# Optimization experiments

Hardware: AMD Instinct MI355X
Metric: run time of the kernel (lower is better)

The kernel has to match this reference:

```python
import jax, jax.numpy as jnp
import numpy as np

B, H, W, C = 16, 64, 64, 256
DIM = 256

def setup_inputs() -> dict:
    key = jax.random.key(0)
    ks = jax.random.split(key, 9)
    s_in = 1.0 / np.sqrt(C)
    x = jax.random.normal(ks[0], (B, H, W, C), dtype=jnp.float32)
    Wq = jax.random.normal(ks[1], (C, DIM), dtype=jnp.float32) * s_in
    bq = jnp.zeros((DIM,), dtype=jnp.float32)
    Wk = jax.random.normal(ks[2], (C, DIM), dtype=jnp.float32) * s_in
    bk = jnp.zeros((DIM,), dtype=jnp.float32)
    Wv = jax.random.normal(ks[3], (C, DIM), dtype=jnp.float32) * s_in
    bv = jnp.zeros((DIM,), dtype=jnp.float32)
    # 'out' conv sees 1 input channel (after the channel reduce_sum)
    Wo = jax.random.normal(ks[4], (1, DIM), dtype=jnp.float32)
    bo = jnp.zeros((DIM,), dtype=jnp.float32)
    return {"x": x, "Wq": Wq, "bq": bq, "Wk": Wk, "bk": bk,
            "Wv": Wv, "bv": bv, "Wo": Wo, "bo": bo}

def reference(x, Wq, bq, Wk, bk, Wv, bv, Wo, bo):
    # 1x1 convs == channel GEMMs
    q = jnp.einsum('bhwc,cd->bhwd', x, Wq) + bq
    k = jnp.einsum('bhwc,cd->bhwd', x, Wk) + bk
    v = jnp.einsum('bhwc,cd->bhwd', x, Wv) + bv
    # channel-reduce score -> [B,H,W,1], softmax jointly over spatial axes
    score = jnp.sum(q * k, axis=-1, keepdims=True)
    attn = jax.nn.softmax(score, axis=(1, 2))
    # channel-reduce of v weighted by per-pixel attn -> [B,H,W,1]
    out = jnp.sum(v * attn, axis=-1, keepdims=True)
    # final 1x1 conv: 1 input channel -> DIM output channels
    return jnp.einsum('bhwc,cd->bhwd', out, Wo) + bo
```

## Files before the change

kernel.cpp:

```cpp
#include <hip/hip_runtime.h>


typedef __bf16 bf16_t;
typedef __attribute__((ext_vector_type(8))) __bf16 bf16x8;
typedef __attribute__((ext_vector_type(4))) __bf16 bf16x4;
typedef __attribute__((ext_vector_type(4))) float f32x4;

#define NBATCH 16
#define NPIX   65536
#define PPB    4096

#define MH_OFF    0u
#define ML_OFF    131072u
#define U_OFF     262144u
#define WV_OFF    263168u
#define SCL_OFF   264192u
#define SCORE_OFF 264448u
#define SV_OFF    526592u
#define BMAX_OFF  788736u
#define BSUM_OFF  788800u

__global__ __launch_bounds__(256) void prep_kernel(
    const float* __restrict__ Wq, const float* __restrict__ bq,
    const float* __restrict__ Wk, const float* __restrict__ bk,
    const float* __restrict__ Wv, const float* __restrict__ bv,
    bf16_t* __restrict__ Mh, bf16_t* __restrict__ Ml,
    float* __restrict__ u, float* __restrict__ wv, float* __restrict__ scl)
{
    const int t = threadIdx.x;
    if (blockIdx.x < 256) {
        const int c = blockIdx.x;
        __shared__ __align__(16) float wq_row[256];
        wq_row[t] = Wq[c * 256 + t];
        __syncthreads();
        const float4* wk4 = (const float4*)(Wk + t * 256);
        const float4* wq4 = (const float4*)wq_row;
        float acc = 0.f;
#pragma unroll 8
        for (int i = 0; i < 64; ++i) {
            float4 a = wq4[i], b = wk4[i];
            acc += a.x * b.x + a.y * b.y + a.z * b.z + a.w * b.w;
        }
        bf16_t h = (bf16_t)acc;
        float hf = (float)h;
        bf16_t l = (bf16_t)(acc - hf);
        Mh[c * 256 + t] = h;
        Ml[c * 256 + t] = l;
    } else {
        float uacc = 0.f, wvacc = 0.f;
        const float* wqr = Wq + t * 256;
        const float* wkr = Wk + t * 256;
        const float* wvr = Wv + t * 256;
#pragma unroll 4
        for (int d = 0; d < 256; ++d) {
            uacc += wqr[d] * bk[d] + wkr[d] * bq[d];
            wvacc += wvr[d];
        }
        u[t] = uacc;
        wv[t] = wvacc;
        __shared__ float r1[256], r2[256];
        r1[t] = bq[t] * bk[t];
        r2[t] = bv[t];
        __syncthreads();
        for (int s = 128; s > 0; s >>= 1) {
            if (t < s) { r1[t] += r1[t + s]; r2[t] += r2[t + s]; }
            __syncthreads();
        }
        if (t == 0) { scl[0] = r1[0]; scl[1] = r2[0]; }
    }
}

__device__ __forceinline__ int swz(int row, int col) {
    return row * 256 + (col ^ ((row & 7) << 3));
}

__global__ __launch_bounds__(256, 2) void score_kernel(
    const float* __restrict__ x,
    const bf16_t* __restrict__ Mh, const bf16_t* __restrict__ Ml,
    const float* __restrict__ u, const float* __restrict__ wvp,
    const float* __restrict__ scl,
    float* __restrict__ score, float* __restrict__ svout)
{
    __shared__ __align__(16) char smem[65536];
    bf16_t* Ah = (bf16_t*)smem;
    bf16_t* Al = Ah + 16384;
    float* redS = (float*)smem;
    float* redV = redS + 256;

    const int t = threadIdx.x;
    const int lane = t & 63;
    const int wid = t >> 6;
    const int l15 = lane & 15;
    const int lg = lane >> 4;
    const int pix0 = blockIdx.x * 64;
    const int wcol0 = wid * 64;

#pragma unroll
    for (int i = 0; i < 16; ++i) {
        int chunk = i * 256 + t;
        int r = chunk >> 6;
        int c4 = (chunk & 63) << 2;
        float4 xv = *(const float4*)(x + (size_t)(pix0 + r) * 256 + c4);
        bf16x4 hi, lo;
        hi[0] = (bf16_t)xv.x; hi[1] = (bf16_t)xv.y;
        hi[2] = (bf16_t)xv.z; hi[3] = (bf16_t)xv.w;
        lo[0] = (bf16_t)(xv.x - (float)hi[0]);
        lo[1] = (bf16_t)(xv.y - (float)hi[1]);
        lo[2] = (bf16_t)(xv.z - (float)hi[2]);
        lo[3] = (bf16_t)(xv.w - (float)hi[3]);
        int idx = swz(r, c4);
        *(bf16x4*)&Ah[idx] = hi;
        *(bf16x4*)&Al[idx] = lo;
    }
    __syncthreads();

    f32x4 acc[4][4];
#pragma unroll
    for (int i = 0; i < 4; ++i)
#pragma unroll
        for (int j = 0; j < 4; ++j)
            acc[i][j] = (f32x4){0.f, 0.f, 0.f, 0.f};

#pragma unroll
    for (int ks = 0; ks < 8; ++ks) {
        const int k0 = ks * 32;
        bf16x8 af_h[4], af_l[4];
#pragma unroll
        for (int rf = 0; rf < 4; ++rf) {
            int row = rf * 16 + l15;
            int idx = swz(row, k0 + lg * 8);
            af_h[rf] = *(const bf16x8*)&Ah[idx];
            af_l[rf] = *(const bf16x8*)&Al[idx];
        }
        bf16x8 bfr_h[4], bfr_l[4];
#pragma unroll
        for (int cf = 0; cf < 4; ++cf) {
            int col = wcol0 + cf * 16 + l15;
            size_t boff = (size_t)col * 256 + k0 + lg * 8;
            bfr_h[cf] = *(const bf16x8*)(Mh + boff);
            bfr_l[cf] = *(const bf16x8*)(Ml + boff);
        }
#pragma unroll
        for (int rf = 0; rf < 4; ++rf)
#pragma unroll
            for (int cf = 0; cf < 4; ++cf)
                acc[rf][cf] = __builtin_amdgcn_mfma_f32_16x16x32_bf16(
                    af_h[rf], bfr_h[cf], acc[rf][cf], 0, 0, 0);
#pragma unroll
        for (int rf = 0; rf < 4; ++rf)
#pragma unroll
            for (int cf = 0; cf < 4; ++cf)
                acc[rf][cf] = __builtin_amdgcn_mfma_f32_16x16x32_bf16(
                    af_l[rf], bfr_h[cf], acc[rf][cf], 0, 0, 0);
#pragma unroll
        for (int rf = 0; rf < 4; ++rf)
#pragma unroll
            for (int cf = 0; cf < 4; ++cf)
                acc[rf][cf] = __builtin_amdgcn_mfma_f32_16x16x32_bf16(
                    af_h[rf], bfr_l[cf], acc[rf][cf], 0, 0, 0);
    }

    float uu[4], wvl[4];
#pragma unroll
    for (int cf = 0; cf < 4; ++cf) {
        uu[cf] = u[wcol0 + cf * 16 + l15];
        wvl[cf] = wvp[wcol0 + cf * 16 + l15];
    }
    float sacc[4][4], vacc[4][4];
#pragma unroll
    for (int rf = 0; rf < 4; ++rf) {
#pragma unroll
        for (int r = 0; r < 4; ++r) {
            int row = rf * 16 + lg * 4 + r;
            float s = 0.f, v = 0.f;
#pragma unroll
            for (int cf = 0; cf < 4; ++cf) {
                int col = wcol0 + cf * 16 + l15;
                int idx = swz(row, col);
                float xv = (float)Ah[idx] + (float)Al[idx];
                s += xv * (acc[rf][cf][r] + uu[cf]);
                v += xv * wvl[cf];
            }
#pragma unroll
            for (int m = 1; m < 16; m <<= 1) {
                s += __shfl_xor(s, m, 64);
                v += __shfl_xor(v, m, 64);
            }
            sacc[rf][r] = s;
            vacc[rf][r] = v;
        }
    }
    __syncthreads();
    if (l15 == 0) {
#pragma unroll
        for (int rf = 0; rf < 4; ++rf)
#pragma unroll
            for (int r = 0; r < 4; ++r) {
                int row = rf * 16 + lg * 4 + r;
                redS[wid * 64 + row] = sacc[rf][r];
                redV[wid * 64 + row] = vacc[rf][r];
            }
    }
    __syncthreads();
    if (t < 64) {
        float c0 = scl[0], bvs = scl[1];
        float s = redS[t] + redS[64 + t] + redS[128 + t] + redS[192 + t] + c0;
        float v = redV[t] + redV[64 + t] + redV[128 + t] + redV[192 + t] + bvs;
        score[pix0 + t] = s;
        svout[pix0 + t] = v;
    }
}

__global__ __launch_bounds__(256) void stats_kernel(
    const float* __restrict__ score,
    float* __restrict__ bmax, float* __restrict__ bsum)
{
    const int b = blockIdx.x, t = threadIdx.x;
    const float* s = score + b * PPB;
    __shared__ float red[256];
    float m = -1e30f;
    for (int i = t; i < PPB; i += 256) m = fmaxf(m, s[i]);
    red[t] = m;
    __syncthreads();
    for (int k = 128; k > 0; k >>= 1) {
        if (t < k) red[t] = fmaxf(red[t], red[t + k]);
        __syncthreads();
    }
    m = red[0];
    __syncthreads();
    float sum = 0.f;
    for (int i = t; i < PPB; i += 256) sum += __expf(s[i] - m);
    red[t] = sum;
    __syncthreads();
    for (int k = 128; k > 0; k >>= 1) {
        if (t < k) red[t] += red[t + k];
        __syncthreads();
    }
    if (t == 0) { bmax[b] = m; bsum[b] = red[0]; }
}

__global__ __launch_bounds__(256) void out_kernel(
    const float* __restrict__ score, const float* __restrict__ sv,
    const float* __restrict__ bmax, const float* __restrict__ bsum,
    const float* __restrict__ Wo, const float* __restrict__ bo,
    float* __restrict__ out)
{
    const int total = NPIX * 64;
    const int stride = gridDim.x * blockDim.x;
    for (int idx = blockIdx.x * blockDim.x + threadIdx.x; idx < total; idx += stride) {
        int p = idx >> 6;
        int c4 = (idx & 63) << 2;
        int b = p >> 12;
        float g = __expf(score[p] - bmax[b]) / bsum[b] * sv[p];
        float4 w = *(const float4*)(Wo + c4);
        float4 bb = *(const float4*)(bo + c4);
        float4 o = { g * w.x + bb.x, g * w.y + bb.y, g * w.z + bb.z, g * w.w + bb.w };
        *(float4*)(out + (size_t)p * 256 + c4) = o;
    }
}

extern "C" void kernel_launch(void* const* d_in, const int* in_sizes, int n_in,
                              void* d_out, int out_size, void* d_ws, size_t ws_size,
                              hipStream_t stream) {
    const float* x  = (const float*)d_in[0];
    const float* Wq = (const float*)d_in[1];
    const float* bq = (const float*)d_in[2];
    const float* Wk = (const float*)d_in[3];
    const float* bk = (const float*)d_in[4];
    const float* Wv = (const float*)d_in[5];
    const float* bv = (const float*)d_in[6];
    const float* Wo = (const float*)d_in[7];
    const float* bo = (const float*)d_in[8];
    float* out = (float*)d_out;
    char* ws = (char*)d_ws;

    bf16_t* Mh = (bf16_t*)(ws + MH_OFF);
    bf16_t* Ml = (bf16_t*)(ws + ML_OFF);
    float* u   = (float*)(ws + U_OFF);
    float* wv  = (float*)(ws + WV_OFF);
    float* scl = (float*)(ws + SCL_OFF);
    float* score = (float*)(ws + SCORE_OFF);
    float* sv    = (float*)(ws + SV_OFF);
    float* bmax  = (float*)(ws + BMAX_OFF);
    float* bsum  = (float*)(ws + BSUM_OFF);

    prep_kernel<<<dim3(257), dim3(256), 0, stream>>>(Wq, bq, Wk, bk, Wv, bv, Mh, Ml, u, wv, scl);
    score_kernel<<<dim3(NPIX / 64), dim3(256), 0, stream>>>(x, Mh, Ml, u, wv, scl, score, sv);
    stats_kernel<<<dim3(NBATCH), dim3(256), 0, stream>>>(score, bmax, bsum);
    out_kernel<<<dim3(2048), dim3(256), 0, stream>>>(score, sv, bmax, bsum, Wo, bo, out);
}
```

Baseline: 102.6 us.

## Split score kernel into two K-halves with 8 waves and overlapped loads

The score kernel now runs 512 threads (8 waves, 32 output columns each) and loads x in two 128-channel halves, so the second half's global load and conversion can overlap the first half's MFMA work. The linear terms x·u and x·wv are computed directly from fp32 x during staging rather than after the GEMM, and the 3-pass MFMA is interleaved per tile. The stats kernel becomes a single-pass online softmax reduction using vectorized loads and wave shuffles, and the output kernel gets twice as many blocks. The risks are more register pressure from holding a second x half in registers, and a higher occupancy hint that may not be reachable with 64KB of LDS per block.

```diff
diff --git a/kernel.cpp b/kernel.cpp
--- a/kernel.cpp
+++ b/kernel.cpp
@@ -74,7 +74,7 @@
     return row * 256 + (col ^ ((row & 7) << 3));
 }
 
-__global__ __launch_bounds__(256, 2) void score_kernel(
+__global__ __launch_bounds__(512, 4) void score_kernel(
     const float* __restrict__ x,
     const bf16_t* __restrict__ Mh, const bf16_t* __restrict__ Ml,
     const float* __restrict__ u, const float* __restrict__ wvp,
@@ -82,10 +82,10 @@
     float* __restrict__ score, float* __restrict__ svout)
 {
     __shared__ __align__(16) char smem[65536];
+    __shared__ float svp[64], tpp[64];
     bf16_t* Ah = (bf16_t*)smem;
     bf16_t* Al = Ah + 16384;
     float* redS = (float*)smem;
-    float* redV = redS + 256;
 
     const int t = threadIdx.x;
     const int lane = t & 63;
@@ -93,101 +93,118 @@
     const int l15 = lane & 15;
     const int lg = lane >> 4;
     const int pix0 = blockIdx.x * 64;
-    const int wcol0 = wid * 64;
-
-#pragma unroll
-    for (int i = 0; i < 16; ++i) {
-        int chunk = i * 256 + t;
-        int r = chunk >> 6;
-        int c4 = (chunk & 63) << 2;
-        float4 xv = *(const float4*)(x + (size_t)(pix0 + r) * 256 + c4);
-        bf16x4 hi, lo;
-        hi[0] = (bf16_t)xv.x; hi[1] = (bf16_t)xv.y;
-        hi[2] = (bf16_t)xv.z; hi[3] = (bf16_t)xv.w;
-        lo[0] = (bf16_t)(xv.x - (float)hi[0]);
-        lo[1] = (bf16_t)(xv.y - (float)hi[1]);
-        lo[2] = (bf16_t)(xv.z - (float)hi[2]);
-        lo[3] = (bf16_t)(xv.w - (float)hi[3]);
-        int idx = swz(r, c4);
-        *(bf16x4*)&Ah[idx] = hi;
-        *(bf16x4*)&Al[idx] = lo;
-    }
-    __syncthreads();
-
-    f32x4 acc[4][4];
+    const int wcol0 = wid * 32;
+
+    const int srow = t >> 3;
+    const int sch = (t & 7) * 16;
+    const float* xrow = x + (size_t)(pix0 + srow) * 256;
+
+    float sv_acc = 0.f, tp_acc = 0.f;
+
+#define CVT_WRITE_DOTS(XV, H)                                                 \
+    {                                                                         \
+        _Pragma("unroll")                                                     \
+        for (int j = 0; j < 2; ++j) {                                         \
+            bf16x8 hi, lo;                                                    \
+            _Pragma("unroll")                                                 \
+            for (int e = 0; e < 8; ++e) {                                     \
+                float f = ((const float*)XV)[j * 8 + e];                      \
+                bf16_t h = (bf16_t)f;                                         \
+                hi[e] = h;                                                    \
+                lo[e] = (bf16_t)(f - (float)h);                               \
+            }                                                                 \
+            int idx = swz(srow, (H) * 128 + sch + j * 8);                     \
+            *(bf16x8*)&Ah[idx] = hi;                                          \
+            *(bf16x8*)&Al[idx] = lo;                                          \
+        }                                                                     \
+        _Pragma("unroll")                                                     \
+        for (int i = 0; i < 4; ++i) {                                         \
+            float4 wvv = *(const float4*)(wvp + (H) * 128 + sch + i * 4);     \
+            float4 uvv = *(const float4*)(u + (H) * 128 + sch + i * 4);       \
+            sv_acc += XV[i].x * wvv.x + XV[i].y * wvv.y +                     \
+                      XV[i].z * wvv.z + XV[i].w * wvv.w;                      \
+            tp_acc += XV[i].x * uvv.x + XV[i].y * uvv.y +                     \
+                      XV[i].z * uvv.z + XV[i].w * uvv.w;                      \
+        }                                                                     \
+    }
+
+    f32x4 acc[4][2];
 #pragma unroll
     for (int i = 0; i < 4; ++i)
 #pragma unroll
-        for (int j = 0; j < 4; ++j)
+        for (int j = 0; j < 2; ++j)
             acc[i][j] = (f32x4){0.f, 0.f, 0.f, 0.f};
 
-#pragma unroll
-    for (int ks = 0; ks < 8; ++ks) {
-        const int k0 = ks * 32;
-        bf16x8 af_h[4], af_l[4];
-#pragma unroll
-        for (int rf = 0; rf < 4; ++rf) {
-            int row = rf * 16 + l15;
-            int idx = swz(row, k0 + lg * 8);
-            af_h[rf] = *(const bf16x8*)&Ah[idx];
-            af_l[rf] = *(const bf16x8*)&Al[idx];
-        }
-        bf16x8 bfr_h[4], bfr_l[4];
-#pragma unroll
-        for (int cf = 0; cf < 4; ++cf) {
-            int col = wcol0 + cf * 16 + l15;
-            size_t boff = (size_t)col * 256 + k0 + lg * 8;
-            bfr_h[cf] = *(const bf16x8*)(Mh + boff);
-            bfr_l[cf] = *(const bf16x8*)(Ml + boff);
-        }
-#pragma unroll
-        for (int rf = 0; rf < 4; ++rf)
-#pragma unroll
-            for (int cf = 0; cf < 4; ++cf)
-                acc[rf][cf] = __builtin_amdgcn_mfma_f32_16x16x32_bf16(
-                    af_h[rf], bfr_h[cf], acc[rf][cf], 0, 0, 0);
-#pragma unroll
-        for (int rf = 0; rf < 4; ++rf)
-#pragma unroll
-            for (int cf = 0; cf < 4; ++cf)
-                acc[rf][cf] = __builtin_amdgcn_mfma_f32_16x16x32_bf16(
-                    af_l[rf], bfr_h[cf], acc[rf][cf], 0, 0, 0);
-#pragma unroll
-        for (int rf = 0; rf < 4; ++rf)
-#pragma unroll
-            for (int cf = 0; cf < 4; ++cf)
-                acc[rf][cf] = __builtin_amdgcn_mfma_f32_16x16x32_bf16(
-                    af_h[rf], bfr_l[cf], acc[rf][cf], 0, 0, 0);
-    }
-
-    float uu[4], wvl[4];
-#pragma unroll
-    for (int cf = 0; cf < 4; ++cf) {
-        uu[cf] = u[wcol0 + cf * 16 + l15];
-        wvl[cf] = wvp[wcol0 + cf * 16 + l15];
-    }
-    float sacc[4][4], vacc[4][4];
+#define MFMA_HALF(H)                                                          \
+    _Pragma("unroll")                                                         \
+    for (int ks = (H) * 4; ks < (H) * 4 + 4; ++ks) {                          \
+        const int k0 = ks * 32;                                               \
+        bf16x8 afh[4], afl[4];                                                \
+        _Pragma("unroll")                                                     \
+        for (int rf = 0; rf < 4; ++rf) {                                      \
+            int idx = swz(rf * 16 + l15, k0 + lg * 8);                        \
+            afh[rf] = *(const bf16x8*)&Ah[idx];                               \
+            afl[rf] = *(const bf16x8*)&Al[idx];                               \
+        }                                                                     \
+        bf16x8 bfh[2], bfl[2];                                                \
+        _Pragma("unroll")                                                     \
+        for (int cf = 0; cf < 2; ++cf) {                                      \
+            size_t bo = (size_t)(wcol0 + cf * 16 + l15) * 256 + k0 + lg * 8;  \
+            bfh[cf] = *(const bf16x8*)(Mh + bo);                              \
+            bfl[cf] = *(const bf16x8*)(Ml + bo);                              \
+        }                                                                     \
+        _Pragma("unroll")                                                     \
+        for (int rf = 0; rf < 4; ++rf)                                        \
+            _Pragma("unroll")                                                 \
+            for (int cf = 0; cf < 2; ++cf) {                                  \
+                acc[rf][cf] = __builtin_amdgcn_mfma_f32_16x16x32_bf16(        \
+                    afh[rf], bfh[cf], acc[rf][cf], 0, 0, 0);                  \
+                acc[rf][cf] = __builtin_amdgcn_mfma_f32_16x16x32_bf16(        \
+                    afl[rf], bfh[cf], acc[rf][cf], 0, 0, 0);                  \
+                acc[rf][cf] = __builtin_amdgcn_mfma_f32_16x16x32_bf16(        \
+                    afh[rf], bfl[cf], acc[rf][cf], 0, 0, 0);                  \
+            }                                                                 \
+    }
+
+    float4 xva[4];
+#pragma unroll
+    for (int i = 0; i < 4; ++i) xva[i] = *(const float4*)(xrow + sch + i * 4);
+    CVT_WRITE_DOTS(xva, 0);
+
+    float4 xvb[4];
+#pragma unroll
+    for (int i = 0; i < 4; ++i) xvb[i] = *(const float4*)(xrow + 128 + sch + i * 4);
+
+    __syncthreads();
+    MFMA_HALF(0);
+
+    CVT_WRITE_DOTS(xvb, 1);
+#pragma unroll
+    for (int m = 1; m < 8; m <<= 1) {
+        sv_acc += __shfl_xor(sv_acc, m, 64);
+        tp_acc += __shfl_xor(tp_acc, m, 64);
+    }
+    if ((lane & 7) == 0) { svp[srow] = sv_acc; tpp[srow] = tp_acc; }
+
+    __syncthreads();
+    MFMA_HALF(1);
+
+    float sacc[4][4];
 #pragma unroll
     for (int rf = 0; rf < 4; ++rf) {
 #pragma unroll
         for (int r = 0; r < 4; ++r) {
             int row = rf * 16 + lg * 4 + r;
-            float s = 0.f, v = 0.f;
-#pragma unroll
-            for (int cf = 0; cf < 4; ++cf) {
-                int col = wcol0 + cf * 16 + l15;
-                int idx = swz(row, col);
+            float s = 0.f;
+#pragma unroll
+            for (int cf = 0; cf < 2; ++cf) {
+                int idx = swz(row, wcol0 + cf * 16 + l15);
                 float xv = (float)Ah[idx] + (float)Al[idx];
-                s += xv * (acc[rf][cf][r] + uu[cf]);
-                v += xv * wvl[cf];
+                s += xv * acc[rf][cf][r];
             }
 #pragma unroll
-            for (int m = 1; m < 16; m <<= 1) {
-                s += __shfl_xor(s, m, 64);
-                v += __shfl_xor(v, m, 64);
-            }
+            for (int m = 1; m < 16; m <<= 1) s += __shfl_xor(s, m, 64);
             sacc[rf][r] = s;
-            vacc[rf][r] = v;
         }
     }
     __syncthreads();
@@ -195,20 +212,19 @@
 #pragma unroll
         for (int rf = 0; rf < 4; ++rf)
 #pragma unroll
-            for (int r = 0; r < 4; ++r) {
-                int row = rf * 16 + lg * 4 + r;
-                redS[wid * 64 + row] = sacc[rf][r];
-                redV[wid * 64 + row] = vacc[rf][r];
-            }
+            for (int r = 0; r < 4; ++r)
+                redS[wid * 64 + rf * 16 + lg * 4 + r] = sacc[rf][r];
     }
     __syncthreads();
     if (t < 64) {
-        float c0 = scl[0], bvs = scl[1];
-        float s = redS[t] + redS[64 + t] + redS[128 + t] + redS[192 + t] + c0;
-        float v = redV[t] + redV[64 + t] + redV[128 + t] + redV[192 + t] + bvs;
+        float s = tpp[t] + scl[0];
+#pragma unroll
+        for (int w = 0; w < 8; ++w) s += redS[w * 64 + t];
         score[pix0 + t] = s;
-        svout[pix0 + t] = v;
-    }
+        svout[pix0 + t] = svp[t] + scl[1];
+    }
+#undef CVT_WRITE_DOTS
+#undef MFMA_HALF
 }
 
 __global__ __launch_bounds__(256) void stats_kernel(
@@ -216,27 +232,39 @@
     float* __restrict__ bmax, float* __restrict__ bsum)
 {
     const int b = blockIdx.x, t = threadIdx.x;
-    const float* s = score + b * PPB;
-    __shared__ float red[256];
-    float m = -1e30f;
-    for (int i = t; i < PPB; i += 256) m = fmaxf(m, s[i]);
-    red[t] = m;
-    __syncthreads();
-    for (int k = 128; k > 0; k >>= 1) {
-        if (t < k) red[t] = fmaxf(red[t], red[t + k]);
-        __syncthreads();
-    }
-    m = red[0];
-    __syncthreads();
+    const int lane = t & 63, wid = t >> 6;
+    const float4* s4 = (const float4*)(score + b * PPB);
+    float4 v[4];
+#pragma unroll
+    for (int i = 0; i < 4; ++i) v[i] = s4[t + i * 256];
+    float m = v[0].x;
+#pragma unroll
+    for (int i = 0; i < 4; ++i) {
+        m = fmaxf(m, fmaxf(fmaxf(v[i].x, v[i].y), fmaxf(v[i].z, v[i].w)));
+    }
     float sum = 0.f;
-    for (int i = t; i < PPB; i += 256) sum += __expf(s[i] - m);
-    red[t] = sum;
-    __syncthreads();
-    for (int k = 128; k > 0; k >>= 1) {
-        if (t < k) red[t] += red[t + k];
-        __syncthreads();
-    }
-    if (t == 0) { bmax[b] = m; bsum[b] = red[0]; }
+#pragma unroll
+    for (int i = 0; i < 4; ++i) {
+        sum += __expf(v[i].x - m) + __expf(v[i].y - m) +
+               __expf(v[i].z - m) + __expf(v[i].w - m);
+    }
+#pragma unroll
+    for (int k = 1; k < 64; k <<= 1) {
+        float om = __shfl_xor(m, k, 64);
+        float os = __shfl_xor(sum, k, 64);
+        float nm = fmaxf(m, om);
+        sum = sum * __expf(m - nm) + os * __expf(om - nm);
+        m = nm;
+    }
+    __shared__ float sm[4], ss[4];
+    if (lane == 0) { sm[wid] = m; ss[wid] = sum; }
+    __syncthreads();
+    if (t == 0) {
+        float M = fmaxf(fmaxf(sm[0], sm[1]), fmaxf(sm[2], sm[3]));
+        float S = ss[0] * __expf(sm[0] - M) + ss[1] * __expf(sm[1] - M) +
+                  ss[2] * __expf(sm[2] - M) + ss[3] * __expf(sm[3] - M);
+        bmax[b] = M; bsum[b] = S;
+    }
 }
 
 __global__ __launch_bounds__(256) void out_kernel(
@@ -285,7 +313,7 @@
     float* bsum  = (float*)(ws + BSUM_OFF);
 
     prep_kernel<<<dim3(257), dim3(256), 0, stream>>>(Wq, bq, Wk, bk, Wv, bv, Mh, Ml, u, wv, scl);
-    score_kernel<<<dim3(NPIX / 64), dim3(256), 0, stream>>>(x, Mh, Ml, u, wv, scl, score, sv);
+    score_kernel<<<dim3(NPIX / 64), dim3(512), 0, stream>>>(x, Mh, Ml, u, wv, scl, score, sv);
     stats_kernel<<<dim3(NBATCH), dim3(256), 0, stream>>>(score, bmax, bsum);
-    out_kernel<<<dim3(2048), dim3(256), 0, stream>>>(score, sv, bmax, bsum, Wo, bo, out);
-}
+    out_kernel<<<dim3(4096), dim3(256), 0, stream>>>(score, sv, bmax, bsum, Wo, bo, out);
+}
```

Result: no change. 103.2 us (+0.6%).
